# Optimization experiments

Measured on AMD Instinct MI355X. Metric: run time of the kernel, lower is better.

The kernel has to match this reference:

```python
import jax, jax.numpy as jnp
import numpy as np

R = 65536          # N_rays
S = 128            # samples per ray
N = R * S          # total samples
L_OP = 0.05        # lambda_opacity (module arg)
L_DIST = 0.001     # lambda_distortion (module arg)
C_RGB = 1.0        # config.lambda_rgb
C_OP = 1.0         # config.lambda_opacity
C_EIK = 0.1        # config.lambda_eikonal


def setup_inputs() -> dict:
    key = jax.random.key(0)
    k = jax.random.split(key, 8)
    rgb = jax.random.uniform(k[0], (R, 3), dtype=jnp.float32)
    target_rays = jax.random.uniform(k[1], (R, 3), dtype=jnp.float32)
    opacity = jax.random.uniform(k[2], (R,), dtype=jnp.float32, minval=1e-4, maxval=1.0)
    grad = jax.random.normal(k[3], (N, 3), dtype=jnp.float32)
    ws = jax.random.uniform(k[4], (N,), dtype=jnp.float32) / S
    deltas = jax.random.uniform(k[5], (N,), dtype=jnp.float32) / S
    # midpoints sorted within each ray segment
    ts = jnp.sort(jax.random.uniform(k[6], (R, S), dtype=jnp.float32), axis=1).reshape(N)
    ray_idx = jax.random.permutation(k[7], R).astype(jnp.int32)
    rays_a = jnp.stack([ray_idx,
                        (jnp.arange(R) * S).astype(jnp.int32),
                        jnp.full((R,), S, dtype=jnp.int32)], axis=1)
    return dict(rgb=rgb, target_rays=target_rays, opacity=opacity, grad=grad,
                ws=ws, deltas=deltas, ts=ts, rays_a=rays_a)


def _smooth_l1(x, y):
    d = jnp.abs(x - y)
    return jnp.mean(jnp.where(d < 1.0, 0.5 * d * d, d - 0.5))


def _distortion_loss(ws, deltas, ts, rays_a):
    # Mip-NeRF 360 distortion via per-segment exclusive prefix sums:
    # loss_r = sum_i 2*w_i*(t_i*W_i^< - WT_i^<) + (1/3) sum_i w_i^2 * delta_i
    n = ws.shape[0]
    n_rays = rays_a.shape[0]
    ray_idx = rays_a[:, 0]
    starts = rays_a[:, 1]                      # sorted ascending (contiguous layout)
    pos = jnp.arange(n)
    seg = jnp.searchsorted(starts, pos, side='right') - 1   # row in rays_a per sample
    cw = jnp.cumsum(ws)
    cwt = jnp.cumsum(ws * ts)
    sm1 = jnp.maximum(starts - 1, 0)
    base_w = jnp.where(starts > 0, cw[sm1], 0.0)
    base_wt = jnp.where(starts > 0, cwt[sm1], 0.0)
    excl_w = cw - ws - base_w[seg]             # exclusive scan of w within segment
    excl_wt = cwt - ws * ts - base_wt[seg]     # exclusive scan of w*t within segment
    per = 2.0 * ws * (ts * excl_w - excl_wt) + ws * ws * deltas / 3.0
    per_row = jax.ops.segment_sum(per, seg, num_segments=n_rays)
    # scatter row losses to their ray index -> (N_rays,)
    return jnp.zeros(n_rays, ws.dtype).at[ray_idx].set(per_row)


def reference(rgb, target_rays, opacity, grad, ws, deltas, ts, rays_a):
    d_rgb = _smooth_l1(rgb, target_rays) * C_RGB
    d_op = L_OP * (-opacity * jnp.log(opacity)) * C_OP          # (N_rays,)
    d_eik = jnp.mean((jnp.linalg.norm(grad, axis=-1) - 1.0) ** 2) * C_EIK
    d_dist = L_DIST * _distortion_loss(ws, deltas, ts, rays_a)  # (N_rays,)
    # pack dict values into one flat array: [rgb, opacity(R), eikonal, distortion(R)]
    return jnp.concatenate([d_rgb[None], d_op, d_eik[None], d_dist])
```

## Files before the change

### kernel.cpp

```cpp
#include <hip/hip_runtime.h>
#include <math.h>

#define R_RAYS 65536
#define S_SAMP 128
#define RAYS_PER_BLOCK 8
#define NB (R_RAYS / RAYS_PER_BLOCK)

template <int CTRL, int ROW_MASK>
__device__ __forceinline__ float dpp_add(float x) {
    int moved = __builtin_amdgcn_update_dpp(0, __float_as_int(x), CTRL, ROW_MASK, 0xF, true);
    return x + __int_as_float(moved);
}

__device__ __forceinline__ float scan32(float x) {
    x = dpp_add<0x111, 0xF>(x);
    x = dpp_add<0x112, 0xF>(x);
    x = dpp_add<0x114, 0xF>(x);
    x = dpp_add<0x118, 0xF>(x);
    x = dpp_add<0x142, 0xA>(x);
    return x;
}

__device__ __forceinline__ float reduce64(float x) {
    x = dpp_add<0x111, 0xF>(x);
    x = dpp_add<0x112, 0xF>(x);
    x = dpp_add<0x114, 0xF>(x);
    x = dpp_add<0x118, 0xF>(x);
    x = dpp_add<0x142, 0xA>(x);
    x = dpp_add<0x143, 0xC>(x);
    return x;
}

__global__ __launch_bounds__(256) void nerf_main_kernel(
    const float* __restrict__ rgb, const float* __restrict__ tgt,
    const float* __restrict__ opacity, const float* __restrict__ grad,
    const float* __restrict__ ws, const float* __restrict__ deltas,
    const float* __restrict__ ts, const int* __restrict__ rays_a,
    float* __restrict__ out, float* __restrict__ partials)
{
    const int tid  = threadIdx.x;
    const int wave = tid >> 6;
    const int lane = tid & 63;
    const int grp  = tid >> 5;
    const int l32  = tid & 31;
    const int b    = blockIdx.x;
    const int r    = b * RAYS_PER_BLOCK + grp;

    const int i0 = r * S_SAMP + l32 * 4;
    const int v0 = r * (S_SAMP / 4) + l32;

    const float4 w4 = ((const float4*)ws)[v0];
    const float4 t4 = ((const float4*)ts)[v0];
    const float4 d4 = ((const float4*)deltas)[v0];
    const float* gp = grad + 3 * i0;
    const float4 g0 = *(const float4*)(gp + 0);
    const float4 g1 = *(const float4*)(gp + 4);
    const float4 g2 = *(const float4*)(gp + 8);
    const int ridx = rays_a[3 * r];

    const float wv[4] = { w4.x, w4.y, w4.z, w4.w };
    const float tv[4] = { t4.x, t4.y, t4.z, t4.w };
    const float dv[4] = { d4.x, d4.y, d4.z, d4.w };

    float wtv[4];
    float sw = 0.f, swt = 0.f;
#pragma unroll
    for (int j = 0; j < 4; ++j) { wtv[j] = wv[j] * tv[j]; sw += wv[j]; swt += wtv[j]; }

    const float isw  = scan32(sw);
    const float iswt = scan32(swt);
    float ew  = isw  - sw;
    float ewt = iswt - swt;

    float per = 0.f;
#pragma unroll
    for (int j = 0; j < 4; ++j) {
        per += 2.f * wv[j] * (tv[j] * ew - ewt) + wv[j] * wv[j] * dv[j] * (1.f / 3.f);
        ew  += wv[j];
        ewt += wtv[j];
    }

    float ek = 0.f;
    {
        float n;
        n = sqrtf(g0.x*g0.x + g0.y*g0.y + g0.z*g0.z); ek += (n-1.f)*(n-1.f);
        n = sqrtf(g0.w*g0.w + g1.x*g1.x + g1.y*g1.y); ek += (n-1.f)*(n-1.f);
        n = sqrtf(g1.z*g1.z + g1.w*g1.w + g2.x*g2.x); ek += (n-1.f)*(n-1.f);
        n = sqrtf(g2.y*g2.y + g2.z*g2.z + g2.w*g2.w); ek += (n-1.f)*(n-1.f);
    }

    const float per_scan = scan32(per);
    const float ek_tot = reduce64(ek);

    __shared__ float s_ek[4], s_rg[8];
    if (lane == 63) s_ek[wave] = ek_tot;

    if (l32 == 31) {
        out[2 + R_RAYS + ridx] = 0.001f * per_scan;
    } else if (l32 == 1) {
        const float op = opacity[r];
        out[1 + r] = 0.05f * (-op * logf(op));
    } else if (l32 == 2) {
        float srgb = 0.f;
#pragma unroll
        for (int c = 0; c < 3; ++c) {
            const float diff = fabsf(rgb[3 * r + c] - tgt[3 * r + c]);
            srgb += (diff < 1.f) ? 0.5f * diff * diff : (diff - 0.5f);
        }
        s_rg[grp] = srgb;
    }
    __syncthreads();

    if (tid == 0) {
        float bek = s_ek[0] + s_ek[1] + s_ek[2] + s_ek[3];
        float brg = 0.f;
#pragma unroll
        for (int j = 0; j < 8; ++j) brg += s_rg[j];
        partials[b]      = bek;
        partials[NB + b] = brg;
    }
}

__global__ __launch_bounds__(1024) void nerf_final_kernel(
    const float* __restrict__ partials, float* __restrict__ out)
{
    const int tid  = threadIdx.x;
    const int lane = tid & 63;
    const int wave = tid >> 6;

    float ek = 0.f, rg = 0.f;
#pragma unroll
    for (int k = 0; k < NB / 1024; ++k) {
        ek += partials[tid + k * 1024];
        rg += partials[NB + tid + k * 1024];
    }
    ek = reduce64(ek);
    rg = reduce64(rg);
    __shared__ float s_ek[16], s_rg[16];
    if (lane == 63) { s_ek[wave] = ek; s_rg[wave] = rg; }
    __syncthreads();
    if (tid == 0) {
        float tek = 0.f, trg = 0.f;
#pragma unroll
        for (int j = 0; j < 16; ++j) { tek += s_ek[j]; trg += s_rg[j]; }
        out[0]          = trg / (3.f * (float)R_RAYS);
        out[1 + R_RAYS] = 0.1f * tek / ((float)R_RAYS * (float)S_SAMP);
    }
}

extern "C" void kernel_launch(void* const* d_in, const int* in_sizes, int n_in,
                              void* d_out, int out_size, void* d_ws, size_t ws_size,
                              hipStream_t stream) {
    const float* rgb     = (const float*)d_in[0];
    const float* tgt     = (const float*)d_in[1];
    const float* opacity = (const float*)d_in[2];
    const float* grad    = (const float*)d_in[3];
    const float* ws      = (const float*)d_in[4];
    const float* deltas  = (const float*)d_in[5];
    const float* ts      = (const float*)d_in[6];
    const int*   rays_a  = (const int*)d_in[7];
    float* out      = (float*)d_out;
    float* partials = (float*)d_ws;

    nerf_main_kernel<<<NB, 256, 0, stream>>>(rgb, tgt, opacity, grad, ws,
                                             deltas, ts, rays_a, out, partials);
    nerf_final_kernel<<<1, 1024, 0, stream>>>(partials, out);
}
```

Measured before the change: 229.4 us.

## Process four rays per wave-half with software-prefetched loads and fewer blocks

```diff
diff --git a/kernel.cpp b/kernel.cpp
--- a/kernel.cpp
+++ b/kernel.cpp
@@ -3,8 +3,9 @@
 
 #define R_RAYS 65536
 #define S_SAMP 128
-#define RAYS_PER_BLOCK 8
-#define NB (R_RAYS / RAYS_PER_BLOCK)
+#define NBLK 2048
+#define GROUPS_PER_BLOCK 8
+#define RAYS_PER_GROUP 4
 
 template <int CTRL, int ROW_MASK>
 __device__ __forceinline__ float dpp_add(float x) {
@@ -44,71 +45,104 @@
     const int grp  = tid >> 5;
     const int l32  = tid & 31;
     const int b    = blockIdx.x;
-    const int r    = b * RAYS_PER_BLOCK + grp;
+    const int gid  = b * GROUPS_PER_BLOCK + grp;
+    const int base = gid * RAYS_PER_GROUP;
 
-    const int i0 = r * S_SAMP + l32 * 4;
-    const int v0 = r * (S_SAMP / 4) + l32;
+    const float4* ws4 = (const float4*)ws;
+    const float4* ts4 = (const float4*)ts;
+    const float4* ds4 = (const float4*)deltas;
 
-    const float4 w4 = ((const float4*)ws)[v0];
-    const float4 t4 = ((const float4*)ts)[v0];
-    const float4 d4 = ((const float4*)deltas)[v0];
-    const float* gp = grad + 3 * i0;
-    const float4 g0 = *(const float4*)(gp + 0);
-    const float4 g1 = *(const float4*)(gp + 4);
-    const float4 g2 = *(const float4*)(gp + 8);
-    const int ridx = rays_a[3 * r];
-
-    const float wv[4] = { w4.x, w4.y, w4.z, w4.w };
-    const float tv[4] = { t4.x, t4.y, t4.z, t4.w };
-    const float dv[4] = { d4.x, d4.y, d4.z, d4.w };
-
-    float wtv[4];
-    float sw = 0.f, swt = 0.f;
+    float srgb = 0.f;
+    int ridx[RAYS_PER_GROUP];
+    if (l32 == 1) {
+        const float4 op4 = *(const float4*)(opacity + base);
+        out[1 + base + 0] = 0.05f * (-op4.x * logf(op4.x));
+        out[1 + base + 1] = 0.05f * (-op4.y * logf(op4.y));
+        out[1 + base + 2] = 0.05f * (-op4.z * logf(op4.z));
+        out[1 + base + 3] = 0.05f * (-op4.w * logf(op4.w));
+    } else if (l32 == 2) {
+        const float* rp = rgb + 3 * base;
+        const float* tp = tgt + 3 * base;
+        const float4 r0 = *(const float4*)(rp + 0), r1 = *(const float4*)(rp + 4), r2 = *(const float4*)(rp + 8);
+        const float4 t0 = *(const float4*)(tp + 0), t1 = *(const float4*)(tp + 4), t2 = *(const float4*)(tp + 8);
+        const float rv[12] = { r0.x,r0.y,r0.z,r0.w, r1.x,r1.y,r1.z,r1.w, r2.x,r2.y,r2.z,r2.w };
+        const float tv_[12] = { t0.x,t0.y,t0.z,t0.w, t1.x,t1.y,t1.z,t1.w, t2.x,t2.y,t2.z,t2.w };
 #pragma unroll
-    for (int j = 0; j < 4; ++j) { wtv[j] = wv[j] * tv[j]; sw += wv[j]; swt += wtv[j]; }
-
-    const float isw  = scan32(sw);
-    const float iswt = scan32(swt);
-    float ew  = isw  - sw;
-    float ewt = iswt - swt;
-
-    float per = 0.f;
-#pragma unroll
-    for (int j = 0; j < 4; ++j) {
-        per += 2.f * wv[j] * (tv[j] * ew - ewt) + wv[j] * wv[j] * dv[j] * (1.f / 3.f);
-        ew  += wv[j];
-        ewt += wtv[j];
+        for (int c = 0; c < 12; ++c) {
+            const float diff = fabsf(rv[c] - tv_[c]);
+            srgb += (diff < 1.f) ? 0.5f * diff * diff : (diff - 0.5f);
+        }
+    } else if (l32 == 31) {
+        const int* ra = rays_a + 3 * base;
+        const int4 q0 = *(const int4*)(ra + 0);
+        const int4 q1 = *(const int4*)(ra + 4);
+        const int4 q2 = *(const int4*)(ra + 8);
+        ridx[0] = q0.x; ridx[1] = q0.w; ridx[2] = q1.z; ridx[3] = q2.y;
     }
 
     float ek = 0.f;
-    {
+
+    int v0 = base * (S_SAMP / 4) + l32;
+    const float* gp = grad + 3 * (base * S_SAMP + l32 * 4);
+    float4 w4c = ws4[v0], t4c = ts4[v0], d4c = ds4[v0];
+    float4 g0c = *(const float4*)(gp + 0);
+    float4 g1c = *(const float4*)(gp + 4);
+    float4 g2c = *(const float4*)(gp + 8);
+
+#pragma unroll
+    for (int it = 0; it < RAYS_PER_GROUP; ++it) {
+        float4 w4n, t4n, d4n, g0n, g1n, g2n;
+        if (it < RAYS_PER_GROUP - 1) {
+            const int vn = (base + it + 1) * (S_SAMP / 4) + l32;
+            const float* gn = grad + 3 * ((base + it + 1) * S_SAMP + l32 * 4);
+            w4n = ws4[vn]; t4n = ts4[vn]; d4n = ds4[vn];
+            g0n = *(const float4*)(gn + 0);
+            g1n = *(const float4*)(gn + 4);
+            g2n = *(const float4*)(gn + 8);
+        }
+
+        const float wv[4] = { w4c.x, w4c.y, w4c.z, w4c.w };
+        const float tv[4] = { t4c.x, t4c.y, t4c.z, t4c.w };
+        const float dv[4] = { d4c.x, d4c.y, d4c.z, d4c.w };
+        float wtv[4];
+        float sw = 0.f, swt = 0.f;
+#pragma unroll
+        for (int j = 0; j < 4; ++j) { wtv[j] = wv[j] * tv[j]; sw += wv[j]; swt += wtv[j]; }
+
+        const float isw  = scan32(sw);
+        const float iswt = scan32(swt);
+        float ew  = isw  - sw;
+        float ewt = iswt - swt;
+
+        float per = 0.f;
+#pragma unroll
+        for (int j = 0; j < 4; ++j) {
+            per += 2.f * wv[j] * (tv[j] * ew - ewt) + wv[j] * wv[j] * dv[j] * (1.f / 3.f);
+            ew  += wv[j];
+            ewt += wtv[j];
+        }
+
         float n;
-        n = sqrtf(g0.x*g0.x + g0.y*g0.y + g0.z*g0.z); ek += (n-1.f)*(n-1.f);
-        n = sqrtf(g0.w*g0.w + g1.x*g1.x + g1.y*g1.y); ek += (n-1.f)*(n-1.f);
-        n = sqrtf(g1.z*g1.z + g1.w*g1.w + g2.x*g2.x); ek += (n-1.f)*(n-1.f);
-        n = sqrtf(g2.y*g2.y + g2.z*g2.z + g2.w*g2.w); ek += (n-1.f)*(n-1.f);
+        n = sqrtf(g0c.x*g0c.x + g0c.y*g0c.y + g0c.z*g0c.z); ek += (n-1.f)*(n-1.f);
+        n = sqrtf(g0c.w*g0c.w + g1c.x*g1c.x + g1c.y*g1c.y); ek += (n-1.f)*(n-1.f);
+        n = sqrtf(g1c.z*g1c.z + g1c.w*g1c.w + g2c.x*g2c.x); ek += (n-1.f)*(n-1.f);
+        n = sqrtf(g2c.y*g2c.y + g2c.z*g2c.z + g2c.w*g2c.w); ek += (n-1.f)*(n-1.f);
+
+        const float per_scan = scan32(per);
+        if (l32 == 31) {
+            out[2 + R_RAYS + ridx[it]] = 0.001f * per_scan;
+        }
+
+        if (it < RAYS_PER_GROUP - 1) {
+            w4c = w4n; t4c = t4n; d4c = d4n;
+            g0c = g0n; g1c = g1n; g2c = g2n;
+        }
     }
 
-    const float per_scan = scan32(per);
     const float ek_tot = reduce64(ek);
-
     __shared__ float s_ek[4], s_rg[8];
     if (lane == 63) s_ek[wave] = ek_tot;
-
-    if (l32 == 31) {
-        out[2 + R_RAYS + ridx] = 0.001f * per_scan;
-    } else if (l32 == 1) {
-        const float op = opacity[r];
-        out[1 + r] = 0.05f * (-op * logf(op));
-    } else if (l32 == 2) {
-        float srgb = 0.f;
-#pragma unroll
-        for (int c = 0; c < 3; ++c) {
-            const float diff = fabsf(rgb[3 * r + c] - tgt[3 * r + c]);
-            srgb += (diff < 1.f) ? 0.5f * diff * diff : (diff - 0.5f);
-        }
-        s_rg[grp] = srgb;
-    }
+    if (l32 == 2)   s_rg[grp]  = srgb;
     __syncthreads();
 
     if (tid == 0) {
@@ -116,8 +150,8 @@
         float brg = 0.f;
 #pragma unroll
         for (int j = 0; j < 8; ++j) brg += s_rg[j];
-        partials[b]      = bek;
-        partials[NB + b] = brg;
+        partials[b]        = bek;
+        partials[NBLK + b] = brg;
     }
 }
 
@@ -128,12 +162,8 @@
     const int lane = tid & 63;
     const int wave = tid >> 6;
 
-    float ek = 0.f, rg = 0.f;
-#pragma unroll
-    for (int k = 0; k < NB / 1024; ++k) {
-        ek += partials[tid + k * 1024];
-        rg += partials[NB + tid + k * 1024];
-    }
+    float ek = partials[tid] + partials[tid + 1024];
+    float rg = partials[NBLK + tid] + partials[NBLK + tid + 1024];
     ek = reduce64(ek);
     rg = reduce64(rg);
     __shared__ float s_ek[16], s_rg[16];
@@ -162,7 +192,7 @@
     float* out      = (float*)d_out;
     float* partials = (float*)d_ws;
 
-    nerf_main_kernel<<<NB, 256, 0, stream>>>(rgb, tgt, opacity, grad, ws,
-                                             deltas, ts, rays_a, out, partials);
+    nerf_main_kernel<<<NBLK, 256, 0, stream>>>(rgb, tgt, opacity, grad, ws,
+                                               deltas, ts, rays_a, out, partials);
     nerf_final_kernel<<<1, 1024, 0, stream>>>(partials, out);
 }
```

Result: no change. 233.7 us (+1.9%).

## Split eikonal reduction into its own kernel with more loads per thread

Applied to the files above, without the earlier changes.

```diff
diff --git a/kernel.cpp b/kernel.cpp
--- a/kernel.cpp
+++ b/kernel.cpp
@@ -3,8 +3,8 @@
 
 #define R_RAYS 65536
 #define S_SAMP 128
-#define RAYS_PER_BLOCK 8
-#define NB (R_RAYS / RAYS_PER_BLOCK)
+#define EIK_BLOCKS 2048
+#define RAY_BLOCKS 8192
 
 template <int CTRL, int ROW_MASK>
 __device__ __forceinline__ float dpp_add(float x) {
@@ -31,31 +31,61 @@
     return x;
 }
 
-__global__ __launch_bounds__(256) void nerf_main_kernel(
+__global__ __launch_bounds__(256) void eik_kernel(
+    const float* __restrict__ grad, float* __restrict__ partials)
+{
+    const int tid  = threadIdx.x;
+    const int wave = tid >> 6;
+    const int lane = tid & 63;
+    const int b    = blockIdx.x;
+
+    const float* gp = grad + (size_t)b * 12288 + wave * 3072 + lane * 12;
+
+    float4 G[12];
+#pragma unroll
+    for (int j = 0; j < 4; ++j) {
+        G[3*j+0] = *(const float4*)(gp + j * 768 + 0);
+        G[3*j+1] = *(const float4*)(gp + j * 768 + 4);
+        G[3*j+2] = *(const float4*)(gp + j * 768 + 8);
+    }
+
+    float ek = 0.f;
+#pragma unroll
+    for (int j = 0; j < 4; ++j) {
+        const float4 g0 = G[3*j+0], g1 = G[3*j+1], g2 = G[3*j+2];
+        float n;
+        n = sqrtf(g0.x*g0.x + g0.y*g0.y + g0.z*g0.z); ek += (n-1.f)*(n-1.f);
+        n = sqrtf(g0.w*g0.w + g1.x*g1.x + g1.y*g1.y); ek += (n-1.f)*(n-1.f);
+        n = sqrtf(g1.z*g1.z + g1.w*g1.w + g2.x*g2.x); ek += (n-1.f)*(n-1.f);
+        n = sqrtf(g2.y*g2.y + g2.z*g2.z + g2.w*g2.w); ek += (n-1.f)*(n-1.f);
+    }
+
+    const float ek_tot = reduce64(ek);
+    __shared__ float s_ek[4];
+    if (lane == 63) s_ek[wave] = ek_tot;
+    __syncthreads();
+    if (tid == 0) partials[b] = s_ek[0] + s_ek[1] + s_ek[2] + s_ek[3];
+}
+
+__global__ __launch_bounds__(256) void ray_kernel(
     const float* __restrict__ rgb, const float* __restrict__ tgt,
-    const float* __restrict__ opacity, const float* __restrict__ grad,
+    const float* __restrict__ opacity,
     const float* __restrict__ ws, const float* __restrict__ deltas,
     const float* __restrict__ ts, const int* __restrict__ rays_a,
     float* __restrict__ out, float* __restrict__ partials)
 {
     const int tid  = threadIdx.x;
-    const int wave = tid >> 6;
-    const int lane = tid & 63;
     const int grp  = tid >> 5;
     const int l32  = tid & 31;
     const int b    = blockIdx.x;
-    const int r    = b * RAYS_PER_BLOCK + grp;
+    const int r    = b * 8 + grp;
 
     const int i0 = r * S_SAMP + l32 * 4;
-    const int v0 = r * (S_SAMP / 4) + l32;
+    const int v0 = i0 >> 2;
 
     const float4 w4 = ((const float4*)ws)[v0];
     const float4 t4 = ((const float4*)ts)[v0];
     const float4 d4 = ((const float4*)deltas)[v0];
-    const float* gp = grad + 3 * i0;
-    const float4 g0 = *(const float4*)(gp + 0);
-    const float4 g1 = *(const float4*)(gp + 4);
-    const float4 g2 = *(const float4*)(gp + 8);
     const int ridx = rays_a[3 * r];
 
     const float wv[4] = { w4.x, w4.y, w4.z, w4.w };
@@ -80,21 +110,9 @@
         ewt += wtv[j];
     }
 
-    float ek = 0.f;
-    {
-        float n;
-        n = sqrtf(g0.x*g0.x + g0.y*g0.y + g0.z*g0.z); ek += (n-1.f)*(n-1.f);
-        n = sqrtf(g0.w*g0.w + g1.x*g1.x + g1.y*g1.y); ek += (n-1.f)*(n-1.f);
-        n = sqrtf(g1.z*g1.z + g1.w*g1.w + g2.x*g2.x); ek += (n-1.f)*(n-1.f);
-        n = sqrtf(g2.y*g2.y + g2.z*g2.z + g2.w*g2.w); ek += (n-1.f)*(n-1.f);
-    }
+    const float per_scan = scan32(per);
 
-    const float per_scan = scan32(per);
-    const float ek_tot = reduce64(ek);
-
-    __shared__ float s_ek[4], s_rg[8];
-    if (lane == 63) s_ek[wave] = ek_tot;
-
+    __shared__ float s_rg[8];
     if (l32 == 31) {
         out[2 + R_RAYS + ridx] = 0.001f * per_scan;
     } else if (l32 == 1) {
@@ -112,12 +130,10 @@
     __syncthreads();
 
     if (tid == 0) {
-        float bek = s_ek[0] + s_ek[1] + s_ek[2] + s_ek[3];
         float brg = 0.f;
 #pragma unroll
         for (int j = 0; j < 8; ++j) brg += s_rg[j];
-        partials[b]      = bek;
-        partials[NB + b] = brg;
+        partials[8192 + b] = brg;
     }
 }
 
@@ -128,12 +144,11 @@
     const int lane = tid & 63;
     const int wave = tid >> 6;
 
-    float ek = 0.f, rg = 0.f;
+    float ek = partials[tid] + partials[tid + 1024];
+    float rg = 0.f;
 #pragma unroll
-    for (int k = 0; k < NB / 1024; ++k) {
-        ek += partials[tid + k * 1024];
-        rg += partials[NB + tid + k * 1024];
-    }
+    for (int k = 0; k < 8; ++k) rg += partials[8192 + tid + k * 1024];
+
     ek = reduce64(ek);
     rg = reduce64(rg);
     __shared__ float s_ek[16], s_rg[16];
@@ -162,7 +177,8 @@
     float* out      = (float*)d_out;
     float* partials = (float*)d_ws;
 
-    nerf_main_kernel<<<NB, 256, 0, stream>>>(rgb, tgt, opacity, grad, ws,
-                                             deltas, ts, rays_a, out, partials);
+    eik_kernel<<<EIK_BLOCKS, 256, 0, stream>>>(grad, partials);
+    ray_kernel<<<RAY_BLOCKS, 256, 0, stream>>>(rgb, tgt, opacity, ws, deltas,
+                                               ts, rays_a, out, partials);
     nerf_final_kernel<<<1, 1024, 0, stream>>>(partials, out);
 }
```

New measurement: 232.0 us. Within noise of the previous version (+1.1%).
